# Performance work log

Hardware: AMD Instinct MI355X
Metric: run time of the kernel (lower is better)

The kernel has to match this reference:

```python
import jax, jax.numpy as jnp
import numpy as np

HEADS1, HID, LSTM_H, OUT = 4, 64, 32, 2
NEG_SLOPE = 0.2
EPS = 1e-16


def gat_layer(x, src, dst, W, att_src, att_dst, bias, heads, out_ch):
    """PyG GATConv (concat=True, add_self_loops handled by caller)."""
    N = x.shape[0]
    h = (x @ W).reshape(N, heads, out_ch)                 # [N, H, C]
    a_s = jnp.sum(h * att_src, axis=-1)                    # [N, H]
    a_d = jnp.sum(h * att_dst, axis=-1)                    # [N, H]
    e = jax.nn.leaky_relu(a_s[src] + a_d[dst], NEG_SLOPE)  # [E, H]
    m = jax.ops.segment_max(e, dst, num_segments=N)        # scatter-softmax (stable)
    e = jnp.exp(e - jax.lax.stop_gradient(m)[dst])
    denom = jax.ops.segment_sum(e, dst, num_segments=N)
    alpha = e / (denom[dst] + EPS)                         # [E, H]
    msg = h[src] * alpha[..., None]                        # [E, H, C]
    out = jax.ops.segment_sum(msg, dst, num_segments=N)    # [N, H, C]
    return out.reshape(N, heads * out_ch) + bias


def lstm_last(seq, W_ih, W_hh, b_ih, b_hh, hidden):
    """Single-layer batch_first LSTM; returns last-step hidden state. Gate order i,f,g,o (torch)."""
    B = seq.shape[0]
    xT = jnp.transpose(seq, (1, 0, 2))  # [T, B, F]
    b = b_ih + b_hh

    def step(carry, xt):
        h, c = carry
        z = xt @ W_ih.T + h @ W_hh.T + b  # [B, 4H]
        i, f, g, o = jnp.split(z, 4, axis=-1)
        c = jax.nn.sigmoid(f) * c + jax.nn.sigmoid(i) * jnp.tanh(g)
        h = jax.nn.sigmoid(o) * jnp.tanh(c)
        return (h, c), None

    h0 = jnp.zeros((B, hidden), seq.dtype)
    (h, _), _ = jax.lax.scan(step, (h0, h0), xT)
    return h


def setup_inputs() -> dict:
    key = jax.random.key(0)
    ks = jax.random.split(key, 20)
    N, E, IN, T = 50000, 800000, 128, 50
    s = lambda k, shp: jax.random.normal(k, shp, jnp.float32) * 0.05
    inp = {
        "x": jax.random.normal(ks[0], (N, IN), jnp.float32),
        "edge_index": jax.random.randint(ks[1], (2, E), 0, N, jnp.int32),
        "sequences": jax.random.normal(ks[2], (N, T, 3), jnp.float32),
        # GATConv 1: in=128 -> 64 per head, 4 heads
        "W1": s(ks[3], (IN, HEADS1 * HID)),
        "att_src1": s(ks[4], (HEADS1, HID)),
        "att_dst1": s(ks[5], (HEADS1, HID)),
        "bias1": jnp.zeros((HEADS1 * HID,), jnp.float32),
        # GATConv 2: in=256 -> 64, 1 head
        "W2": s(ks[6], (HEADS1 * HID, HID)),
        "att_src2": s(ks[7], (1, HID)),
        "att_dst2": s(ks[8], (1, HID)),
        "bias2": jnp.zeros((HID,), jnp.float32),
        # LSTM(input_size=3, hidden_size=32)
        "W_ih": s(ks[9], (4 * LSTM_H, 3)),
        "W_hh": s(ks[10], (4 * LSTM_H, LSTM_H)),
        "b_ih": jnp.zeros((4 * LSTM_H,), jnp.float32),
        "b_hh": jnp.zeros((4 * LSTM_H,), jnp.float32),
        # fusion MLP: (64+32) -> 64 -> 2
        "Wf1": s(ks[11], (HID + LSTM_H, HID)),
        "bf1": jnp.zeros((HID,), jnp.float32),
        "Wf2": s(ks[12], (HID, OUT)),
        "bf2": jnp.zeros((OUT,), jnp.float32),
    }
    return inp


def reference(x, edge_index, sequences, W1, att_src1, att_dst1, bias1,
              W2, att_src2, att_dst2, bias2, W_ih, W_hh, b_ih, b_hh,
              Wf1, bf1, Wf2, bf2):
    N = x.shape[0]
    # PyG GATConv default add_self_loops=True
    loops = jnp.arange(N, dtype=edge_index.dtype)
    src = jnp.concatenate([edge_index[0], loops])
    dst = jnp.concatenate([edge_index[1], loops])

    g = jax.nn.elu(gat_layer(x, src, dst, W1, att_src1, att_dst1, bias1, HEADS1, HID))
    # dropout is identity in eval mode
    g = gat_layer(g, src, dst, W2, att_src2, att_dst2, bias2, 1, HID)  # [N, 64]

    t = lstm_last(sequences, W_ih, W_hh, b_ih, b_hh, LSTM_H)           # [N, 32]

    combined = jnp.concatenate([g, t], axis=1)
    h = jax.nn.relu(combined @ Wf1 + bf1)
    return h @ Wf2 + bf2
```

## Files before the change

kernel.cpp:

```cpp
#include <hip/hip_runtime.h>
#include <math.h>

#define HEADS1 4
#define HID 64
#define LSTM_H 32
#define IN_F 128
#define T_STEPS 50
#define NEG_SLOPE 0.2f
#define EPS_A 1e-16f

typedef __attribute__((ext_vector_type(8))) short short8;
typedef __attribute__((ext_vector_type(4))) float floatx4;
typedef __attribute__((ext_vector_type(4))) unsigned uint32x4;

__device__ __forceinline__ float frcp(float x) {
    float r;
    asm("v_rcp_f32 %0, %1" : "=v"(r) : "v"(x));
    return r;
}
__device__ __forceinline__ float sigf(float x) { return frcp(1.0f + __expf(-x)); }
__device__ __forceinline__ float tanhfast(float x) {
    float e = __expf(2.0f * x);
    return 1.0f - 2.0f * frcp(e + 1.0f);
}
__device__ __forceinline__ unsigned short f2bf(float f) {
    unsigned u = __float_as_uint(f);
    unsigned r = (u + 0x7FFFu + ((u >> 16) & 1u)) >> 16;
    return (unsigned short)r;
}
__device__ __forceinline__ float bf2f(unsigned short s) {
    return __uint_as_float(((unsigned)s) << 16);
}
__device__ __forceinline__ unsigned cvt_pk_bf16(float a, float b) {
    unsigned r;
    asm("v_cvt_pk_bf16_f32 %0, %1, %2" : "=v"(r) : "v"(a), "v"(b));
    return r;
}
__device__ __forceinline__ float lo16f(unsigned p) { return __uint_as_float(p << 16); }
__device__ __forceinline__ float hi16f(unsigned p) { return __uint_as_float(p & 0xffff0000u); }
__device__ __forceinline__ short8 bc8(uint32x4 v) { return __builtin_bit_cast(short8, v); }

template <int KK>
__global__ void prep_wt(const float* __restrict__ W, unsigned short* __restrict__ th,
                        unsigned short* __restrict__ tl, int total, int NC) {
    int i = blockIdx.x * 256 + threadIdx.x;
    if (i >= total) return;
    int n = i / KK, k = i - n * KK;
    float v = W[k * NC + n];
    unsigned short h = f2bf(v);
    th[i] = h;
    tl[i] = f2bf(v - bf2f(h));
}

template <int K, int NC>
__global__ __launch_bounds__(256)
void gemm_mfma(const float* __restrict__ A, const unsigned short* __restrict__ Bth,
               const unsigned short* __restrict__ Btl, float* __restrict__ C, int M) {
    __shared__ float sA[128][44];
    __shared__ unsigned short sBh[64][40];
    __shared__ unsigned short sBl[64][40];
    const int tid = threadIdx.x;
    const int wave = tid >> 6, lane = tid & 63;
    const int wr = wave >> 1, wc = wave & 1;
    const int row0 = blockIdx.x * 128;
    const int col0 = blockIdx.y * 64;
    const int l15 = lane & 15, l4 = lane >> 4;

    floatx4 acc[4][2];
#pragma unroll
    for (int rb = 0; rb < 4; rb++)
#pragma unroll
        for (int cb = 0; cb < 2; cb++) acc[rb][cb] = (floatx4){0.f, 0.f, 0.f, 0.f};

    for (int k0 = 0; k0 < K; k0 += 32) {
        __syncthreads();
#pragma unroll
        for (int q = 0; q < 4; q++) {
            int idx = q * 256 + tid;
            int row = idx >> 3, seg = idx & 7;
            int gr = row0 + row;
            float4 v = (gr < M) ? *(const float4*)&A[(size_t)gr * K + k0 + seg * 4]
                                : make_float4(0.f, 0.f, 0.f, 0.f);
            *(float4*)&sA[row][seg * 4] = v;
        }
        {
            int col = tid >> 2, seg = tid & 3;
            size_t gb = (size_t)(col0 + col) * K + k0 + seg * 8;
            *(short8*)&sBh[col][seg * 8] = *(const short8*)&Bth[gb];
            *(short8*)&sBl[col][seg * 8] = *(const short8*)&Btl[gb];
        }
        __syncthreads();

        short8 bh0 = *(const short8*)&sBh[wc * 32 + 0 + l15][l4 * 8];
        short8 bl0 = *(const short8*)&sBl[wc * 32 + 0 + l15][l4 * 8];
        short8 bh1 = *(const short8*)&sBh[wc * 32 + 16 + l15][l4 * 8];
        short8 bl1 = *(const short8*)&sBl[wc * 32 + 16 + l15][l4 * 8];

#pragma unroll
        for (int rb = 0; rb < 4; rb++) {
            int row = wr * 64 + rb * 16 + l15;
            floatx4 a0 = *(const floatx4*)&sA[row][l4 * 8 + 0];
            floatx4 a1 = *(const floatx4*)&sA[row][l4 * 8 + 4];
            unsigned p0 = cvt_pk_bf16(a0[0], a0[1]);
            unsigned p1 = cvt_pk_bf16(a0[2], a0[3]);
            unsigned p2 = cvt_pk_bf16(a1[0], a1[1]);
            unsigned p3 = cvt_pk_bf16(a1[2], a1[3]);
            uint32x4 hp = {p0, p1, p2, p3};
            short8 Ah = bc8(hp);
            unsigned q0 = cvt_pk_bf16(a0[0] - lo16f(p0), a0[1] - hi16f(p0));
            unsigned q1 = cvt_pk_bf16(a0[2] - lo16f(p1), a0[3] - hi16f(p1));
            unsigned q2 = cvt_pk_bf16(a1[0] - lo16f(p2), a1[1] - hi16f(p2));
            unsigned q3 = cvt_pk_bf16(a1[2] - lo16f(p3), a1[3] - hi16f(p3));
            uint32x4 lp = {q0, q1, q2, q3};
            short8 Al = bc8(lp);

            acc[rb][0] = __builtin_amdgcn_mfma_f32_16x16x32_bf16(Ah, bh0, acc[rb][0], 0, 0, 0);
            acc[rb][0] = __builtin_amdgcn_mfma_f32_16x16x32_bf16(Ah, bl0, acc[rb][0], 0, 0, 0);
            acc[rb][0] = __builtin_amdgcn_mfma_f32_16x16x32_bf16(Al, bh0, acc[rb][0], 0, 0, 0);
            acc[rb][1] = __builtin_amdgcn_mfma_f32_16x16x32_bf16(Ah, bh1, acc[rb][1], 0, 0, 0);
            acc[rb][1] = __builtin_amdgcn_mfma_f32_16x16x32_bf16(Ah, bl1, acc[rb][1], 0, 0, 0);
            acc[rb][1] = __builtin_amdgcn_mfma_f32_16x16x32_bf16(Al, bh1, acc[rb][1], 0, 0, 0);
        }
    }

#pragma unroll
    for (int rb = 0; rb < 4; rb++)
#pragma unroll
        for (int cb = 0; cb < 2; cb++)
#pragma unroll
            for (int q = 0; q < 4; q++) {
                int row = row0 + wr * 64 + rb * 16 + l4 * 4 + q;
                int col = col0 + wc * 32 + cb * 16 + l15;
                if (row < M) C[(size_t)row * NC + col] = acc[rb][cb][q];
            }
}

__global__ void att_scores(const float* __restrict__ h, const float* __restrict__ att_s,
                           const float* __restrict__ att_d, float* __restrict__ as_,
                           float* __restrict__ ad_, int NH, int Hmask) {
    int i = blockIdx.x * blockDim.x + threadIdx.x;
    if (i >= NH) return;
    int hh = i & Hmask;
    const float* row = h + (size_t)i * HID;
    float s = 0.0f, d = 0.0f;
#pragma unroll 8
    for (int c = 0; c < HID; c++) {
        float v = row[c];
        s += v * att_s[hh * HID + c];
        d += v * att_d[hh * HID + c];
    }
    as_[i] = s;
    ad_[i] = d;
}

__global__ void count_deg(const int* __restrict__ dsts, int E, int ET, int* __restrict__ cnt) {
    int e = blockIdx.x * blockDim.x + threadIdx.x;
    if (e >= ET) return;
    int d = (e < E) ? dsts[e] : (e - E);
    atomicAdd(&cnt[d], 1);
}

__global__ void scan1(const int* __restrict__ cnt, int* __restrict__ rowp,
                      int* __restrict__ bsum, int N) {
    __shared__ int tmp[256];
    int i = blockIdx.x * 256 + threadIdx.x;
    int v = (i < N) ? cnt[i] : 0;
    tmp[threadIdx.x] = v;
    __syncthreads();
    for (int off = 1; off < 256; off <<= 1) {
        int t = (threadIdx.x >= (unsigned)off) ? tmp[threadIdx.x - off] : 0;
        __syncthreads();
        tmp[threadIdx.x] += t;
        __syncthreads();
    }
    if (i < N) rowp[i] = tmp[threadIdx.x] - v;
    if (threadIdx.x == 255) bsum[blockIdx.x] = tmp[255];
}

__global__ void scan2(int* __restrict__ bsum, int nb) {
    __shared__ int tmp[256];
    int v = (threadIdx.x < (unsigned)nb) ? bsum[threadIdx.x] : 0;
    tmp[threadIdx.x] = v;
    __syncthreads();
    for (int off = 1; off < 256; off <<= 1) {
        int t = (threadIdx.x >= (unsigned)off) ? tmp[threadIdx.x - off] : 0;
        __syncthreads();
        tmp[threadIdx.x] += t;
        __syncthreads();
    }
    if (threadIdx.x < (unsigned)nb) bsum[threadIdx.x] = tmp[threadIdx.x] - v;
}

__global__ void scan3(int* __restrict__ rowp, const int* __restrict__ bsum, int N, int ET) {
    int i = blockIdx.x * 256 + threadIdx.x;
    if (i < N) rowp[i] += bsum[blockIdx.x];
    if (i == 0) rowp[N] = ET;
}

__global__ void scatter_edges(const int* __restrict__ dsts, int E, int ET,
                              const int* __restrict__ rowp, int* __restrict__ cursor,
                              int* __restrict__ eid) {
    int e = blockIdx.x * blockDim.x + threadIdx.x;
    if (e >= ET) return;
    int d = (e < E) ? dsts[e] : (e - E);
    int pos = atomicAdd(&cursor[d], 1);
    eid[rowp[d] + pos] = e;
}

__global__ __launch_bounds__(256)
void gat_agg4_sp(const int* __restrict__ srcs, int E,
                 const int* __restrict__ rowp, const int* __restrict__ eid,
                 const float* __restrict__ as_, const float* __restrict__ ad_,
                 const float* __restrict__ hfeat, const float* __restrict__ bias,
                 float* __restrict__ g, int N) {
    __shared__ float s_alpha[4][64][4];
    const int wave = threadIdx.x >> 6;
    const int lane = threadIdx.x & 63;
    const int head = lane >> 4;
    const int dst = blockIdx.x * 4 + wave;
    if (dst >= N) return;
    const int start = rowp[dst], end = rowp[dst + 1];
    const float4 adv = ((const float4*)ad_)[dst];
    const float4* h4 = (const float4*)hfeat;

    float4 dsum = make_float4(0.f, 0.f, 0.f, 0.f);
    float4 acc  = make_float4(0.f, 0.f, 0.f, 0.f);

    for (int i0 = start; i0 < end; i0 += 64) {
        int cnt = min(64, end - i0);
        int i = i0 + lane;
        int s = 0;
        if (i < end) {
            int e = eid[i];
            s = (e < E) ? srcs[e] : (e - E);
            float4 a = ((const float4*)as_)[s];
            float tx, ex;
            tx = a.x + adv.x; tx = (tx > 0.f) ? tx : NEG_SLOPE * tx; ex = __expf(tx);
            dsum.x += ex; s_alpha[wave][lane][0] = ex;
            tx = a.y + adv.y; tx = (tx > 0.f) ? tx : NEG_SLOPE * tx; ex = __expf(tx);
            dsum.y += ex; s_alpha[wave][lane][1] = ex;
            tx = a.z + adv.z; tx = (tx > 0.f) ? tx : NEG_SLOPE * tx; ex = __expf(tx);
            dsum.z += ex; s_alpha[wave][lane][2] = ex;
            tx = a.w + adv.w; tx = (tx > 0.f) ? tx : NEG_SLOPE * tx; ex = __expf(tx);
            dsum.w += ex; s_alpha[wave][lane][3] = ex;
        }
        __builtin_amdgcn_wave_barrier();
#pragma unroll 4
        for (int k = 0; k < cnt; k++) {
            float a_k = s_alpha[wave][k][head];
            int   s_k = __shfl(s, k);
            float4 hv = h4[(size_t)s_k * 64 + lane];
            acc.x += a_k * hv.x; acc.y += a_k * hv.y;
            acc.z += a_k * hv.z; acc.w += a_k * hv.w;
        }
        __builtin_amdgcn_wave_barrier();
    }
#pragma unroll
    for (int mk = 32; mk >= 1; mk >>= 1) {
        dsum.x += __shfl_xor(dsum.x, mk);
        dsum.y += __shfl_xor(dsum.y, mk);
        dsum.z += __shfl_xor(dsum.z, mk);
        dsum.w += __shfl_xor(dsum.w, mk);
    }
    float den = (head == 0) ? dsum.x : (head == 1) ? dsum.y : (head == 2) ? dsum.z : dsum.w;
    float inv = 1.0f / (den + EPS_A);
    float4 b4 = ((const float4*)bias)[lane];
    float4 r;
    r.x = acc.x * inv + b4.x; r.x = (r.x > 0.f) ? r.x : __expf(r.x) - 1.f;
    r.y = acc.y * inv + b4.y; r.y = (r.y > 0.f) ? r.y : __expf(r.y) - 1.f;
    r.z = acc.z * inv + b4.z; r.z = (r.z > 0.f) ? r.z : __expf(r.z) - 1.f;
    r.w = acc.w * inv + b4.w; r.w = (r.w > 0.f) ? r.w : __expf(r.w) - 1.f;
    ((float4*)g)[(size_t)dst * 64 + lane] = r;
}

__global__ __launch_bounds__(256)
void gat_agg1_sp(const int* __restrict__ srcs, int E,
                 const int* __restrict__ rowp, const int* __restrict__ eid,
                 const float* __restrict__ as_, const float* __restrict__ ad_,
                 const float* __restrict__ hfeat, const float* __restrict__ bias,
                 float* __restrict__ g, int N) {
    __shared__ float s_alpha[4][64];
    const int wave = threadIdx.x >> 6;
    const int lane = threadIdx.x & 63;
    const int dst = blockIdx.x * 4 + wave;
    if (dst >= N) return;
    const int start = rowp[dst], end = rowp[dst + 1];
    const float adv = ad_[dst];

    float dsum = 0.0f, acc = 0.0f;
    for (int i0 = start; i0 < end; i0 += 64) {
        int cnt = min(64, end - i0);
        int i = i0 + lane;
        int s = 0;
        if (i < end) {
            int e = eid[i];
            s = (e < E) ? srcs[e] : (e - E);
            float t = as_[s] + adv;
            t = (t > 0.f) ? t : NEG_SLOPE * t;
            float ex = __expf(t);
            dsum += ex;
            s_alpha[wave][lane] = ex;
        }
        __builtin_amdgcn_wave_barrier();
#pragma unroll 4
        for (int k = 0; k < cnt; k++) {
            float a_k = s_alpha[wave][k];
            int   s_k = __shfl(s, k);
            acc += a_k * hfeat[(size_t)s_k * 64 + lane];
        }
        __builtin_amdgcn_wave_barrier();
    }
#pragma unroll
    for (int mk = 32; mk >= 1; mk >>= 1) dsum += __shfl_xor(dsum, mk);
    g[(size_t)dst * 64 + lane] = acc / (dsum + EPS_A) + bias[lane];
}

__global__ void prep_wsplit(const float* __restrict__ Wih, const float* __restrict__ Whh,
                            const float* __restrict__ bih, const float* __restrict__ bhh,
                            uint32x4* __restrict__ wsp) {
    const int tid = threadIdx.x;
    const int kk = tid >> 7, sub = (tid >> 6) & 1, lane = tid & 63;
    const int grp = lane >> 4, col = lane & 15;
    const int krow = grp * 8;
    const int n = (sub + kk * 2) * 16 + col;
    float w[8];
    *(float4*)&w[0] = *(const float4*)&Whh[n * 32 + krow + 0];
    *(float4*)&w[4] = *(const float4*)&Whh[n * 32 + krow + 4];
    unsigned hi[8], lo[8];
#pragma unroll
    for (int j = 0; j < 8; j++) {
        unsigned short hs = f2bf(w[j]);
        hi[j] = hs;
        lo[j] = f2bf(w[j] - bf2f(hs));
    }
    uint32x4 BH = {hi[0] | (hi[1] << 16), hi[2] | (hi[3] << 16),
                   hi[4] | (hi[5] << 16), hi[6] | (hi[7] << 16)};
    uint32x4 BL = {lo[0] | (lo[1] << 16), lo[2] | (lo[3] << 16),
                   lo[4] | (lo[5] << 16), lo[6] | (lo[7] << 16)};
    float wi0 = Wih[n * 3 + 0], wi1 = Wih[n * 3 + 1], wi2 = Wih[n * 3 + 2];
    float bb = bih[n] + bhh[n];
    unsigned h0 = f2bf(wi0), h1 = f2bf(wi1), h2 = f2bf(wi2), hb = f2bf(bb);
    uint32x4 B2 = {0u, 0u, 0u, 0u};
    if (grp == 0) {
        unsigned bl_ = f2bf(bb - bf2f((unsigned short)hb));
        B2[0] = h0 | (h1 << 16); B2[1] = h2 | (hb << 16);
        B2[2] = h0 | (h1 << 16); B2[3] = h2 | (bl_ << 16);
    } else if (grp == 1) {
        unsigned l0 = f2bf(wi0 - bf2f((unsigned short)h0));
        unsigned l1 = f2bf(wi1 - bf2f((unsigned short)h1));
        unsigned l2 = f2bf(wi2 - bf2f((unsigned short)h2));
        B2[0] = l0 | (l1 << 16); B2[1] = l2;
    }
    wsp[((kk * 3 + 0) * 2 + sub) * 64 + lane] = B2;
    wsp[((kk * 3 + 1) * 2 + sub) * 64 + lane] = BH;
    wsp[((kk * 3 + 2) * 2 + sub) * 64 + lane] = BL;
}

__global__ __launch_bounds__(512)
void lstm_mfma(const float* __restrict__ seq, const uint32x4* __restrict__ wsp,
               float* __restrict__ t_out, int N) {
    __shared__ float s_h[4][2][16][36];

    const int tid  = threadIdx.x;
    const int wave = tid >> 6, lane = tid & 63;
    const int pair = wave >> 1, sub = wave & 1;
    const int grp  = lane >> 4, col = lane & 15;
    const int node0 = blockIdx.x * 64 + pair * 16;

#define LF(KK, W) wsp[(((KK) * 3 + (W)) * 2 + sub) * 64 + lane]
    uint32x4 B2_0 = LF(0, 0), BH_0 = LF(0, 1), BL_0 = LF(0, 2);
    uint32x4 B2_1 = LF(1, 0), BH_1 = LF(1, 1), BL_1 = LF(1, 2);
    uint32x4 B2_2 = LF(2, 0), BH_2 = LF(2, 1), BL_2 = LF(2, 2);
    uint32x4 B2_3 = LF(3, 0), BH_3 = LF(3, 1), BL_3 = LF(3, 2);
#undef LF
    asm volatile("" : "+v"(B2_0), "+v"(BH_0), "+v"(BL_0),
                      "+v"(B2_1), "+v"(BH_1), "+v"(BL_1),
                      "+v"(B2_2), "+v"(BH_2), "+v"(BL_2),
                      "+v"(B2_3), "+v"(BH_3), "+v"(BL_3));

    for (int i = tid; i < 4 * 2 * 16 * 36; i += 512) ((float*)s_h)[i] = 0.0f;
    __syncthreads();

    float cst0 = 0.f, cst1 = 0.f, cst2 = 0.f, cst3 = 0.f;
    float hn0 = 0.f, hn1 = 0.f, hn2 = 0.f, hn3 = 0.f;
    const floatx4 zac = {0.f, 0.f, 0.f, 0.f};

    const int nodeX = node0 + col;
    const bool vx = (nodeX < N) && (grp < 2);
    const bool g0 = (grp == 0);
    const float* xp = seq + (size_t)nodeX * (T_STEPS * 3);

    float xv0 = vx ? xp[0] : 0.0f;
    float xv1 = vx ? xp[1] : 0.0f;
    float xv2 = vx ? xp[2] : 0.0f;

#pragma unroll 1
    for (int t = 0; t < T_STEPS; t++) {
        unsigned w0 = cvt_pk_bf16(xv0, xv1);
        unsigned w1 = cvt_pk_bf16(xv2, g0 ? 1.0f : 0.0f);
        float e0 = xv0 - lo16f(w0);
        float e1 = xv1 - hi16f(w0);
        float e2 = xv2 - lo16f(w1);
        unsigned w2 = g0 ? cvt_pk_bf16(e0, e1) : 0u;
        unsigned w3 = g0 ? cvt_pk_bf16(e2, 1.0f) : 0u;
        uint32x4 a2p = {w0, w1, w2, w3};
        short8 A2 = bc8(a2p);

        const float* hr = &s_h[pair][(t + 1) & 1][col][grp * 8];
        floatx4 h0 = *(const floatx4*)&hr[0];
        floatx4 h1 = *(const floatx4*)&hr[4];
        unsigned p0 = cvt_pk_bf16(h0[0], h0[1]);
        unsigned p1 = cvt_pk_bf16(h0[2], h0[3]);
        unsigned p2 = cvt_pk_bf16(h1[0], h1[1]);
        unsigned p3 = cvt_pk_bf16(h1[2], h1[3]);
        uint32x4 hip = {p0, p1, p2, p3};
        short8 Ahi = bc8(hip);
        unsigned q0 = cvt_pk_bf16(h0[0] - lo16f(p0), h0[1] - hi16f(p0));
        unsigned q1 = cvt_pk_bf16(h0[2] - lo16f(p1), h0[3] - hi16f(p1));
        unsigned q2 = cvt_pk_bf16(h1[0] - lo16f(p2), h1[1] - hi16f(p2));
        unsigned q3 = cvt_pk_bf16(h1[2] - lo16f(p3), h1[3] - hi16f(p3));
        uint32x4 lop = {q0, q1, q2, q3};
        short8 Alo = bc8(lop);

        {
            int tn = (t + 1 < T_STEPS) ? (t + 1) : t;
            xv0 = vx ? xp[tn * 3 + 0] : 0.0f;
            xv1 = vx ? xp[tn * 3 + 1] : 0.0f;
            xv2 = vx ? xp[tn * 3 + 2] : 0.0f;
        }

        floatx4 d0 = __builtin_amdgcn_mfma_f32_16x16x32_bf16(A2, bc8(B2_0), zac, 0, 0, 0);
        d0 = __builtin_amdgcn_mfma_f32_16x16x32_bf16(Alo, bc8(BH_0), d0, 0, 0, 0);
        d0 = __builtin_amdgcn_mfma_f32_16x16x32_bf16(Ahi, bc8(BL_0), d0, 0, 0, 0);
        d0 = __builtin_amdgcn_mfma_f32_16x16x32_bf16(Ahi, bc8(BH_0), d0, 0, 0, 0);
        floatx4 d1 = __builtin_amdgcn_mfma_f32_16x16x32_bf16(A2, bc8(B2_1), zac, 0, 0, 0);
        d1 = __builtin_amdgcn_mfma_f32_16x16x32_bf16(Alo, bc8(BH_1), d1, 0, 0, 0);
        d1 = __builtin_amdgcn_mfma_f32_16x16x32_bf16(Ahi, bc8(BL_1), d1, 0, 0, 0);
        d1 = __builtin_amdgcn_mfma_f32_16x16x32_bf16(Ahi, bc8(BH_1), d1, 0, 0, 0);
        floatx4 d2 = __builtin_amdgcn_mfma_f32_16x16x32_bf16(A2, bc8(B2_2), zac, 0, 0, 0);
        d2 = __builtin_amdgcn_mfma_f32_16x16x32_bf16(Alo, bc8(BH_2), d2, 0, 0, 0);
        d2 = __builtin_amdgcn_mfma_f32_16x16x32_bf16(Ahi, bc8(BL_2), d2, 0, 0, 0);
        d2 = __builtin_amdgcn_mfma_f32_16x16x32_bf16(Ahi, bc8(BH_2), d2, 0, 0, 0);
        floatx4 d3 = __builtin_amdgcn_mfma_f32_16x16x32_bf16(A2, bc8(B2_3), zac, 0, 0, 0);
        d3 = __builtin_amdgcn_mfma_f32_16x16x32_bf16(Alo, bc8(BH_3), d3, 0, 0, 0);
        d3 = __builtin_amdgcn_mfma_f32_16x16x32_bf16(Ahi, bc8(BL_3), d3, 0, 0, 0);
        d3 = __builtin_amdgcn_mfma_f32_16x16x32_bf16(Ahi, bc8(BH_3), d3, 0, 0, 0);

        {
            float ig, fg, gv, og;
            ig = sigf(d0[0]); fg = sigf(d1[0]); gv = tanhfast(d2[0]); og = sigf(d3[0]);
            cst0 = fg * cst0 + ig * gv; hn0 = og * tanhfast(cst0);
            ig = sigf(d0[1]); fg = sigf(d1[1]); gv = tanhfast(d2[1]); og = sigf(d3[1]);
            cst1 = fg * cst1 + ig * gv; hn1 = og * tanhfast(cst1);
            ig = sigf(d0[2]); fg = sigf(d1[2]); gv = tanhfast(d2[2]); og = sigf(d3[2]);
            cst2 = fg * cst2 + ig * gv; hn2 = og * tanhfast(cst2);
            ig = sigf(d0[3]); fg = sigf(d1[3]); gv = tanhfast(d2[3]); og = sigf(d3[3]);
            cst3 = fg * cst3 + ig * gv; hn3 = og * tanhfast(cst3);
        }

        float* hw = &s_h[pair][t & 1][4 * grp][sub * 16 + col];
        hw[0 * 36] = hn0; hw[1 * 36] = hn1; hw[2 * 36] = hn2; hw[3 * 36] = hn3;
        __syncthreads();
    }

    {
        int node = node0 + 4 * grp;
        const int c = sub * 16 + col;
        if (node + 0 < N) t_out[(size_t)(node + 0) * LSTM_H + c] = hn0;
        if (node + 1 < N) t_out[(size_t)(node + 1) * LSTM_H + c] = hn1;
        if (node + 2 < N) t_out[(size_t)(node + 2) * LSTM_H + c] = hn2;
        if (node + 3 < N) t_out[(size_t)(node + 3) * LSTM_H + c] = hn3;
    }
}

__global__ void fusion_kernel(const float* __restrict__ g2, const float* __restrict__ tt,
                              const float* __restrict__ Wf1, const float* __restrict__ bf1,
                              const float* __restrict__ Wf2, const float* __restrict__ bf2,
                              float* __restrict__ out, int N) {
    __shared__ float sW[96 * 64];
    __shared__ float sb1[64];
    __shared__ float sW2[128];
    for (int i = threadIdx.x; i < 96 * 64; i += 256) sW[i] = Wf1[i];
    if (threadIdx.x < 64) sb1[threadIdx.x] = bf1[threadIdx.x];
    if (threadIdx.x < 128) sW2[threadIdx.x] = Wf2[threadIdx.x];
    __syncthreads();
    const int wave = threadIdx.x >> 6;
    const int lane = threadIdx.x & 63;
    for (int n = blockIdx.x * 4 + wave; n < N; n += gridDim.x * 4) {
        const float* gn = g2 + (size_t)n * 64;
        const float* tn = tt + (size_t)n * 32;
        float acc = sb1[lane];
#pragma unroll 8
        for (int k = 0; k < 64; k++) acc += gn[k] * sW[k * 64 + lane];
#pragma unroll 8
        for (int k = 0; k < 32; k++) acc += tn[k] * sW[(64 + k) * 64 + lane];
        acc = fmaxf(acc, 0.0f);
        float o0 = acc * sW2[lane * 2 + 0];
        float o1 = acc * sW2[lane * 2 + 1];
#pragma unroll
        for (int mk = 32; mk >= 1; mk >>= 1) {
            o0 += __shfl_xor(o0, mk);
            o1 += __shfl_xor(o1, mk);
        }
        if (lane == 0) {
            out[(size_t)n * 2 + 0] = o0 + bf2[0];
            out[(size_t)n * 2 + 1] = o1 + bf2[1];
        }
    }
}

extern "C" void kernel_launch(void* const* d_in, const int* in_sizes, int n_in,
                              void* d_out, int out_size, void* d_ws, size_t ws_size,
                              hipStream_t stream) {
    const float* x      = (const float*)d_in[0];
    const int*   eidx   = (const int*)d_in[1];
    const float* seq    = (const float*)d_in[2];
    const float* W1     = (const float*)d_in[3];
    const float* att_s1 = (const float*)d_in[4];
    const float* att_d1 = (const float*)d_in[5];
    const float* bias1  = (const float*)d_in[6];
    const float* W2     = (const float*)d_in[7];
    const float* att_s2 = (const float*)d_in[8];
    const float* att_d2 = (const float*)d_in[9];
    const float* bias2  = (const float*)d_in[10];
    const float* Wih    = (const float*)d_in[11];
    const float* Whh    = (const float*)d_in[12];
    const float* bih    = (const float*)d_in[13];
    const float* bhh    = (const float*)d_in[14];
    const float* Wf1    = (const float*)d_in[15];
    const float* bf1    = (const float*)d_in[16];
    const float* Wf2    = (const float*)d_in[17];
    const float* bf2    = (const float*)d_in[18];
    float* out = (float*)d_out;

    const int N  = in_sizes[0] / IN_F;
    const int E  = in_sizes[1] / 2;
    const int ET = E + N;
    const int* srcs = eidx;
    const int* dsts = eidx + E;

    float* fws = (float*)d_ws;
    size_t o = 0;
    float* h1  = fws + o; o += (size_t)N * 256;
    float* g1  = fws + o; o += (size_t)N * 256;
    float* as1 = fws + o; o += (size_t)N * 4;
    float* ad1 = fws + o; o += (size_t)N * 4;
    int* cnt    = (int*)(fws + o);
    int* rowp   = cnt + N;
    int* cursor = rowp + N + 1;
    int* eid    = cursor + N;
    int* bsum   = eid + ET;
    uintptr_t wp_ = (uintptr_t)(bsum + 512);
    wp_ = (wp_ + 15) & ~(uintptr_t)15;
    uint32x4* wsp = (uint32x4*)wp_;
    unsigned short* w1h = (unsigned short*)(wsp + 1536);
    unsigned short* w1l = w1h + 32768;
    unsigned short* w2h = w1l + 32768;
    unsigned short* w2l = w2h + 16384;
    float* h2 = h1;
    float* g2 = h1 + (size_t)N * 64;
    float* tt = h1 + (size_t)N * 128;
    float* as2 = as1; float* ad2 = ad1;

    const int nTiles = (N + 255) / 256;
    dim3 blk(256);

    hipMemsetAsync(cnt, 0, (size_t)N * sizeof(int), stream);
    hipMemsetAsync(cursor, 0, (size_t)N * sizeof(int), stream);
    count_deg<<<(ET + 255) / 256, blk, 0, stream>>>(dsts, E, ET, cnt);
    scan1<<<nTiles, blk, 0, stream>>>(cnt, rowp, bsum, N);
    scan2<<<1, blk, 0, stream>>>(bsum, nTiles);
    scan3<<<(N + 256) / 256, blk, 0, stream>>>(rowp, bsum, N, ET);
    scatter_edges<<<(ET + 255) / 256, blk, 0, stream>>>(dsts, E, ET, rowp, cursor, eid);

    prep_wsplit<<<1, 512, 0, stream>>>(Wih, Whh, bih, bhh, wsp);
    prep_wt<128><<<(32768 + 255) / 256, blk, 0, stream>>>(W1, w1h, w1l, 32768, 256);
    prep_wt<256><<<(16384 + 255) / 256, blk, 0, stream>>>(W2, w2h, w2l, 16384, 64);

    gemm_mfma<128, 256><<<dim3((N + 127) / 128, 4), blk, 0, stream>>>(x, w1h, w1l, h1, N);
    att_scores<<<(N * 4 + 255) / 256, blk, 0, stream>>>(h1, att_s1, att_d1, as1, ad1, N * 4, 3);
    gat_agg4_sp<<<(N + 3) / 4, blk, 0, stream>>>(srcs, E, rowp, eid, as1, ad1, h1, bias1, g1, N);

    lstm_mfma<<<(N + 63) / 64, dim3(512), 0, stream>>>(seq, wsp, tt, N);

    gemm_mfma<256, 64><<<dim3((N + 127) / 128, 1), blk, 0, stream>>>(g1, w2h, w2l, h2, N);
    att_scores<<<(N + 255) / 256, blk, 0, stream>>>(h2, att_s2, att_d2, as2, ad2, N, 0);
    gat_agg1_sp<<<(N + 3) / 4, blk, 0, stream>>>(srcs, E, rowp, eid, as2, ad2, h2, bias2, g2, N);

    fusion_kernel<<<512, blk, 0, stream>>>(g2, tt, Wf1, bf1, Wf2, bf2, out, N);
}
```

Measured before the change: 726.7 us.

## Compute all LSTM hidden columns per wave, replacing block barriers with wave barriers

Each wave now computes all 32 hidden units for its 16 nodes instead of splitting them across a wave pair. The recurrent state therefore stays within one wave, so the per-step __syncthreads and the double-buffered shared state become single-buffer wave barriers. In exchange each wave issues twice the MFMAs per step and holds twice the weight fragments in registers (24 uint32x4). Block size drops to 256, and the register pressure may lower occupancy.

```diff
diff --git a/kernel.cpp b/kernel.cpp
--- a/kernel.cpp
+++ b/kernel.cpp
@@ -356,33 +356,34 @@
     wsp[((kk * 3 + 2) * 2 + sub) * 64 + lane] = BL;
 }
 
-__global__ __launch_bounds__(512)
+__global__ __launch_bounds__(256)
 void lstm_mfma(const float* __restrict__ seq, const uint32x4* __restrict__ wsp,
                float* __restrict__ t_out, int N) {
-    __shared__ float s_h[4][2][16][36];
+    __shared__ float s_h[4][16][36];
 
     const int tid  = threadIdx.x;
     const int wave = tid >> 6, lane = tid & 63;
-    const int pair = wave >> 1, sub = wave & 1;
     const int grp  = lane >> 4, col = lane & 15;
-    const int node0 = blockIdx.x * 64 + pair * 16;
-
-#define LF(KK, W) wsp[(((KK) * 3 + (W)) * 2 + sub) * 64 + lane]
-    uint32x4 B2_0 = LF(0, 0), BH_0 = LF(0, 1), BL_0 = LF(0, 2);
-    uint32x4 B2_1 = LF(1, 0), BH_1 = LF(1, 1), BL_1 = LF(1, 2);
-    uint32x4 B2_2 = LF(2, 0), BH_2 = LF(2, 1), BL_2 = LF(2, 2);
-    uint32x4 B2_3 = LF(3, 0), BH_3 = LF(3, 1), BL_3 = LF(3, 2);
+    const int node0 = blockIdx.x * 64 + wave * 16;
+
+#define LF(KK, W, HF) wsp[(((KK) * 3 + (W)) * 2 + (HF)) * 64 + lane]
+    uint32x4 B2_i0 = LF(0, 0, 0), BH_i0 = LF(0, 1, 0), BL_i0 = LF(0, 2, 0);
+    uint32x4 B2_i1 = LF(0, 0, 1), BH_i1 = LF(0, 1, 1), BL_i1 = LF(0, 2, 1);
+    uint32x4 B2_f0 = LF(1, 0, 0), BH_f0 = LF(1, 1, 0), BL_f0 = LF(1, 2, 0);
+    uint32x4 B2_f1 = LF(1, 0, 1), BH_f1 = LF(1, 1, 1), BL_f1 = LF(1, 2, 1);
+    uint32x4 B2_g0 = LF(2, 0, 0), BH_g0 = LF(2, 1, 0), BL_g0 = LF(2, 2, 0);
+    uint32x4 B2_g1 = LF(2, 0, 1), BH_g1 = LF(2, 1, 1), BL_g1 = LF(2, 2, 1);
+    uint32x4 B2_o0 = LF(3, 0, 0), BH_o0 = LF(3, 1, 0), BL_o0 = LF(3, 2, 0);
+    uint32x4 B2_o1 = LF(3, 0, 1), BH_o1 = LF(3, 1, 1), BL_o1 = LF(3, 2, 1);
 #undef LF
-    asm volatile("" : "+v"(B2_0), "+v"(BH_0), "+v"(BL_0),
-                      "+v"(B2_1), "+v"(BH_1), "+v"(BL_1),
-                      "+v"(B2_2), "+v"(BH_2), "+v"(BL_2),
-                      "+v"(B2_3), "+v"(BH_3), "+v"(BL_3));
-
-    for (int i = tid; i < 4 * 2 * 16 * 36; i += 512) ((float*)s_h)[i] = 0.0f;
-    __syncthreads();
-
-    float cst0 = 0.f, cst1 = 0.f, cst2 = 0.f, cst3 = 0.f;
-    float hn0 = 0.f, hn1 = 0.f, hn2 = 0.f, hn3 = 0.f;
+
+    for (int i = lane; i < 16 * 36; i += 64) (&s_h[wave][0][0])[i] = 0.0f;
+    __builtin_amdgcn_wave_barrier();
+
+    float cA0 = 0.f, cA1 = 0.f, cA2 = 0.f, cA3 = 0.f;
+    float cB0 = 0.f, cB1 = 0.f, cB2 = 0.f, cB3 = 0.f;
+    float hA0 = 0.f, hA1 = 0.f, hA2 = 0.f, hA3 = 0.f;
+    float hB0 = 0.f, hB1 = 0.f, hB2 = 0.f, hB3 = 0.f;
     const floatx4 zac = {0.f, 0.f, 0.f, 0.f};
 
     const int nodeX = node0 + col;
@@ -406,7 +407,7 @@
         uint32x4 a2p = {w0, w1, w2, w3};
         short8 A2 = bc8(a2p);
 
-        const float* hr = &s_h[pair][(t + 1) & 1][col][grp * 8];
+        const float* hr = &s_h[wave][col][grp * 8];
         floatx4 h0 = *(const floatx4*)&hr[0];
         floatx4 h1 = *(const floatx4*)&hr[4];
         unsigned p0 = cvt_pk_bf16(h0[0], h0[1]);
@@ -429,47 +430,66 @@
             xv2 = vx ? xp[tn * 3 + 2] : 0.0f;
         }
 
-        floatx4 d0 = __builtin_amdgcn_mfma_f32_16x16x32_bf16(A2, bc8(B2_0), zac, 0, 0, 0);
-        d0 = __builtin_amdgcn_mfma_f32_16x16x32_bf16(Alo, bc8(BH_0), d0, 0, 0, 0);
-        d0 = __builtin_amdgcn_mfma_f32_16x16x32_bf16(Ahi, bc8(BL_0), d0, 0, 0, 0);
-        d0 = __builtin_amdgcn_mfma_f32_16x16x32_bf16(Ahi, bc8(BH_0), d0, 0, 0, 0);
-        floatx4 d1 = __builtin_amdgcn_mfma_f32_16x16x32_bf16(A2, bc8(B2_1), zac, 0, 0, 0);
-        d1 = __builtin_amdgcn_mfma_f32_16x16x32_bf16(Alo, bc8(BH_1), d1, 0, 0, 0);
-        d1 = __builtin_amdgcn_mfma_f32_16x16x32_bf16(Ahi, bc8(BL_1), d1, 0, 0, 0);
-        d1 = __builtin_amdgcn_mfma_f32_16x16x32_bf16(Ahi, bc8(BH_1), d1, 0, 0, 0);
-        floatx4 d2 = __builtin_amdgcn_mfma_f32_16x16x32_bf16(A2, bc8(B2_2), zac, 0, 0, 0);
-        d2 = __builtin_amdgcn_mfma_f32_16x16x32_bf16(Alo, bc8(BH_2), d2, 0, 0, 0);
-        d2 = __builtin_amdgcn_mfma_f32_16x16x32_bf16(Ahi, bc8(BL_2), d2, 0, 0, 0);
-        d2 = __builtin_amdgcn_mfma_f32_16x16x32_bf16(Ahi, bc8(BH_2), d2, 0, 0, 0);
-        floatx4 d3 = __builtin_amdgcn_mfma_f32_16x16x32_bf16(A2, bc8(B2_3), zac, 0, 0, 0);
-        d3 = __builtin_amdgcn_mfma_f32_16x16x32_bf16(Alo, bc8(BH_3), d3, 0, 0, 0);
-        d3 = __builtin_amdgcn_mfma_f32_16x16x32_bf16(Ahi, bc8(BL_3), d3, 0, 0, 0);
-        d3 = __builtin_amdgcn_mfma_f32_16x16x32_bf16(Ahi, bc8(BH_3), d3, 0, 0, 0);
+#define GBLK(D, B2V, BHV, BLV)                                                   \
+        floatx4 D = __builtin_amdgcn_mfma_f32_16x16x32_bf16(A2, bc8(B2V), zac, 0, 0, 0); \
+        D = __builtin_amdgcn_mfma_f32_16x16x32_bf16(Alo, bc8(BHV), D, 0, 0, 0);  \
+        D = __builtin_amdgcn_mfma_f32_16x16x32_bf16(Ahi, bc8(BLV), D, 0, 0, 0);  \
+        D = __builtin_amdgcn_mfma_f32_16x16x32_bf16(Ahi, bc8(BHV), D, 0, 0, 0);
+        GBLK(di0, B2_i0, BH_i0, BL_i0)
+        GBLK(di1, B2_i1, BH_i1, BL_i1)
+        GBLK(df0, B2_f0, BH_f0, BL_f0)
+        GBLK(df1, B2_f1, BH_f1, BL_f1)
+        GBLK(dg0, B2_g0, BH_g0, BL_g0)
+        GBLK(dg1, B2_g1, BH_g1, BL_g1)
+        GBLK(do0, B2_o0, BH_o0, BL_o0)
+        GBLK(do1, B2_o1, BH_o1, BL_o1)
+#undef GBLK
 
         {
             float ig, fg, gv, og;
-            ig = sigf(d0[0]); fg = sigf(d1[0]); gv = tanhfast(d2[0]); og = sigf(d3[0]);
-            cst0 = fg * cst0 + ig * gv; hn0 = og * tanhfast(cst0);
-            ig = sigf(d0[1]); fg = sigf(d1[1]); gv = tanhfast(d2[1]); og = sigf(d3[1]);
-            cst1 = fg * cst1 + ig * gv; hn1 = og * tanhfast(cst1);
-            ig = sigf(d0[2]); fg = sigf(d1[2]); gv = tanhfast(d2[2]); og = sigf(d3[2]);
-            cst2 = fg * cst2 + ig * gv; hn2 = og * tanhfast(cst2);
-            ig = sigf(d0[3]); fg = sigf(d1[3]); gv = tanhfast(d2[3]); og = sigf(d3[3]);
-            cst3 = fg * cst3 + ig * gv; hn3 = og * tanhfast(cst3);
-        }
-
-        float* hw = &s_h[pair][t & 1][4 * grp][sub * 16 + col];
-        hw[0 * 36] = hn0; hw[1 * 36] = hn1; hw[2 * 36] = hn2; hw[3 * 36] = hn3;
-        __syncthreads();
+            ig = sigf(di0[0]); fg = sigf(df0[0]); gv = tanhfast(dg0[0]); og = sigf(do0[0]);
+            cA0 = fg * cA0 + ig * gv; hA0 = og * tanhfast(cA0);
+            ig = sigf(di0[1]); fg = sigf(df0[1]); gv = tanhfast(dg0[1]); og = sigf(do0[1]);
+            cA1 = fg * cA1 + ig * gv; hA1 = og * tanhfast(cA1);
+            ig = sigf(di0[2]); fg = sigf(df0[2]); gv = tanhfast(dg0[2]); og = sigf(do0[2]);
+            cA2 = fg * cA2 + ig * gv; hA2 = og * tanhfast(cA2);
+            ig = sigf(di0[3]); fg = sigf(df0[3]); gv = tanhfast(dg0[3]); og = sigf(do0[3]);
+            cA3 = fg * cA3 + ig * gv; hA3 = og * tanhfast(cA3);
+            ig = sigf(di1[0]); fg = sigf(df1[0]); gv = tanhfast(dg1[0]); og = sigf(do1[0]);
+            cB0 = fg * cB0 + ig * gv; hB0 = og * tanhfast(cB0);
+            ig = sigf(di1[1]); fg = sigf(df1[1]); gv = tanhfast(dg1[1]); og = sigf(do1[1]);
+            cB1 = fg * cB1 + ig * gv; hB1 = og * tanhfast(cB1);
+            ig = sigf(di1[2]); fg = sigf(df1[2]); gv = tanhfast(dg1[2]); og = sigf(do1[2]);
+            cB2 = fg * cB2 + ig * gv; hB2 = og * tanhfast(cB2);
+            ig = sigf(di1[3]); fg = sigf(df1[3]); gv = tanhfast(dg1[3]); og = sigf(do1[3]);
+            cB3 = fg * cB3 + ig * gv; hB3 = og * tanhfast(cB3);
+        }
+
+        __builtin_amdgcn_wave_barrier();
+        {
+            float* hw = &s_h[wave][4 * grp][0];
+            hw[0 * 36 + col]      = hA0;
+            hw[1 * 36 + col]      = hA1;
+            hw[2 * 36 + col]      = hA2;
+            hw[3 * 36 + col]      = hA3;
+            hw[0 * 36 + 16 + col] = hB0;
+            hw[1 * 36 + 16 + col] = hB1;
+            hw[2 * 36 + 16 + col] = hB2;
+            hw[3 * 36 + 16 + col] = hB3;
+        }
+        __builtin_amdgcn_wave_barrier();
     }
 
     {
         int node = node0 + 4 * grp;
-        const int c = sub * 16 + col;
-        if (node + 0 < N) t_out[(size_t)(node + 0) * LSTM_H + c] = hn0;
-        if (node + 1 < N) t_out[(size_t)(node + 1) * LSTM_H + c] = hn1;
-        if (node + 2 < N) t_out[(size_t)(node + 2) * LSTM_H + c] = hn2;
-        if (node + 3 < N) t_out[(size_t)(node + 3) * LSTM_H + c] = hn3;
+        if (node + 0 < N) { t_out[(size_t)(node + 0) * LSTM_H + col] = hA0;
+                            t_out[(size_t)(node + 0) * LSTM_H + 16 + col] = hB0; }
+        if (node + 1 < N) { t_out[(size_t)(node + 1) * LSTM_H + col] = hA1;
+                            t_out[(size_t)(node + 1) * LSTM_H + 16 + col] = hB1; }
+        if (node + 2 < N) { t_out[(size_t)(node + 2) * LSTM_H + col] = hA2;
+                            t_out[(size_t)(node + 2) * LSTM_H + 16 + col] = hB2; }
+        if (node + 3 < N) { t_out[(size_t)(node + 3) * LSTM_H + col] = hA3;
+                            t_out[(size_t)(node + 3) * LSTM_H + 16 + col] = hB3; }
     }
 }
 
@@ -581,7 +601,7 @@
     att_scores<<<(N * 4 + 255) / 256, blk, 0, stream>>>(h1, att_s1, att_d1, as1, ad1, N * 4, 3);
     gat_agg4_sp<<<(N + 3) / 4, blk, 0, stream>>>(srcs, E, rowp, eid, as1, ad1, h1, bias1, g1, N);
 
-    lstm_mfma<<<(N + 63) / 64, dim3(512), 0, stream>>>(seq, wsp, tt, N);
+    lstm_mfma<<<(N + 63) / 64, dim3(256), 0, stream>>>(seq, wsp, tt, N);
 
     gemm_mfma<256, 64><<<dim3((N + 127) / 128, 1), blk, 0, stream>>>(g1, w2h, w2l, h2, N);
     att_scores<<<(N + 255) / 256, blk, 0, stream>>>(h2, att_s2, att_d2, as2, ad2, N, 0);
```

After: 737.3 us. No clear change (+1.5%).
